# Optimization experiments

Measured on AMD Instinct MI355X. Metric: run time of the kernel, lower is better.

## Reference

```python
import jax, jax.numpy as jnp
import numpy as np

D_MODEL = 512
NUM_HEADS = 8


def setup_inputs() -> dict:
    key = jax.random.key(0)
    ks = jax.random.split(key, 12)
    B, S, D = 2, 4096, D_MODEL
    s = 1.0 / np.sqrt(D)
    return {
        "q": jax.random.normal(ks[0], (B, S, D), jnp.float32),
        "k": jax.random.normal(ks[1], (B, S, D), jnp.float32),
        "v": jax.random.normal(ks[2], (B, S, D), jnp.float32),
        "w_q": jax.random.normal(ks[3], (D, D), jnp.float32) * s,
        "b_q": jax.random.normal(ks[4], (D,), jnp.float32) * s,
        "w_k": jax.random.normal(ks[5], (D, D), jnp.float32) * s,
        "b_k": jax.random.normal(ks[6], (D,), jnp.float32) * s,
        "w_v": jax.random.normal(ks[7], (D, D), jnp.float32) * s,
        "b_v": jax.random.normal(ks[8], (D,), jnp.float32) * s,
        "w_o": jax.random.normal(ks[9], (D, D), jnp.float32) * s,
        "b_o": jax.random.normal(ks[10], (D,), jnp.float32) * s,
    }


def _split(x, num_heads):
    B, S, D = x.shape
    return x.reshape(B, S, num_heads, D // num_heads).transpose(0, 2, 1, 3)


def reference(q, k, v, w_q, b_q, w_k, b_k, w_v, b_v, w_o, b_o):
    # Linear projections (torch Linear: x @ W^T + b)
    qp = q @ w_q.T + b_q
    kp = k @ w_k.T + b_k
    vp = v @ w_v.T + b_v
    # split into heads: [B, H, S, d_head]
    qh = _split(qp, NUM_HEADS)
    kh = _split(kp, NUM_HEADS)
    vh = _split(vp, NUM_HEADS)
    d_head = qh.shape[-1]
    # NOTE: original scales by sqrt(d_model of the per-head tensor) == sqrt(d_head)
    score = jnp.einsum("bhqd,bhkd->bhqk", qh, kh) / jnp.sqrt(jnp.float32(d_head))
    attn = jax.nn.softmax(score, axis=-1)  # full [B,H,S,S] materialized, as in source
    out = jnp.einsum("bhqk,bhkd->bhqd", attn, vh)
    # concat heads back to [B, S, D]
    B, H, S, Dh = out.shape
    out = out.transpose(0, 2, 1, 3).reshape(B, S, H * Dh)
    return out @ w_o.T + b_o
```

## Files before the change

### kernel.cpp

```cpp
#include <hip/hip_runtime.h>
#include <math.h>

typedef __bf16 bf16_t;
typedef __bf16 bf16x4_v __attribute__((ext_vector_type(4)));
typedef __bf16 bf16x8_t __attribute__((ext_vector_type(8)));
typedef float f32x4_t __attribute__((ext_vector_type(4)));
typedef short short4_t __attribute__((ext_vector_type(4)));
typedef unsigned uint2_t __attribute__((ext_vector_type(2)));

#define S_LEN 4096
#define DM 512
#define NH 8
#define DH 64
#define MTOT 8192

#define Q_SCALE 0.1803368801111204f

__device__ inline f32x4_t mfma16(bf16x8_t a, bf16x8_t b, f32x4_t c) {
    return __builtin_amdgcn_mfma_f32_16x16x32_bf16(a, b, c, 0, 0, 0);
}

__device__ inline f32x4_t mfma_pv(short4_t a, short4_t b, f32x4_t c) {
    return __builtin_amdgcn_mfma_f32_16x16x16bf16_1k(a, b, c, 0, 0, 0);
}

__device__ inline unsigned pkbf16(float a, float b) {
    unsigned short ra = __builtin_bit_cast(unsigned short, (bf16_t)a);
    unsigned short rb = __builtin_bit_cast(unsigned short, (bf16_t)b);
    return (unsigned)ra | ((unsigned)rb << 16);
}

__device__ inline void async_copy16(const void* g, void* l) {
    __builtin_amdgcn_global_load_lds(
        (const __attribute__((address_space(1))) void*)g,
        (__attribute__((address_space(3))) void*)l, 16, 0, 0);
}

__global__ __launch_bounds__(256) void gemm_qkv(
    const float* __restrict__ X0, const float* __restrict__ X1, const float* __restrict__ X2,
    const float* __restrict__ W0, const float* __restrict__ W1, const float* __restrict__ W2,
    const float* __restrict__ B0, const float* __restrict__ B1, const float* __restrict__ B2,
    bf16_t* __restrict__ dst_base)
{
    const int p = blockIdx.z;
    const float* __restrict__ X  = (p == 0) ? X0 : ((p == 1) ? X1 : X2);
    const float* __restrict__ W  = (p == 0) ? W0 : ((p == 1) ? W1 : W2);
    const float* __restrict__ Bi = (p == 0) ? B0 : ((p == 1) ? B1 : B2);
    bf16_t* __restrict__ dst = dst_base + (size_t)p * (size_t)MTOT * DM;

    const int m0 = blockIdx.x * 128;
    const int n0 = blockIdx.y * 128;
    const int tid = threadIdx.x;
    const int lane = tid & 63, wid = tid >> 6;
    const int lm = lane & 15, lg = lane >> 4;
    const int wm = (wid >> 1) * 64, wn = (wid & 1) * 64;

    __shared__ bf16_t As[128][40];
    __shared__ bf16_t Bs[128][40];

    f32x4_t acc[4][4] = {};

    for (int kb = 0; kb < DM / 32; ++kb) {
        const int k0 = kb * 32;
#pragma unroll
        for (int i = 0; i < 2; ++i) {
            int idx = i * 256 + tid;
            int r = idx >> 2;
            int c = (idx & 3) * 8;
            const float* sa = X + (size_t)(m0 + r) * DM + k0 + c;
            float4 a0 = *(const float4*)sa;
            float4 a1 = *(const float4*)(sa + 4);
            bf16x8_t ha;
            ha[0] = (bf16_t)a0.x; ha[1] = (bf16_t)a0.y; ha[2] = (bf16_t)a0.z; ha[3] = (bf16_t)a0.w;
            ha[4] = (bf16_t)a1.x; ha[5] = (bf16_t)a1.y; ha[6] = (bf16_t)a1.z; ha[7] = (bf16_t)a1.w;
            *(bf16x8_t*)&As[r][c] = ha;
            const float* sb = W + (size_t)(n0 + r) * DM + k0 + c;
            float4 b0 = *(const float4*)sb;
            float4 b1 = *(const float4*)(sb + 4);
            bf16x8_t hb;
            hb[0] = (bf16_t)b0.x; hb[1] = (bf16_t)b0.y; hb[2] = (bf16_t)b0.z; hb[3] = (bf16_t)b0.w;
            hb[4] = (bf16_t)b1.x; hb[5] = (bf16_t)b1.y; hb[6] = (bf16_t)b1.z; hb[7] = (bf16_t)b1.w;
            *(bf16x8_t*)&Bs[r][c] = hb;
        }
        __syncthreads();
        bf16x8_t fa[4], fb[4];
#pragma unroll
        for (int mt = 0; mt < 4; ++mt) fa[mt] = *(bf16x8_t*)&As[wm + mt * 16 + lm][lg * 8];
#pragma unroll
        for (int nt = 0; nt < 4; ++nt) fb[nt] = *(bf16x8_t*)&Bs[wn + nt * 16 + lm][lg * 8];
#pragma unroll
        for (int mt = 0; mt < 4; ++mt)
#pragma unroll
            for (int nt = 0; nt < 4; ++nt)
                acc[mt][nt] = mfma16(fa[mt], fb[nt], acc[mt][nt]);
        __syncthreads();
    }

    if (p == 2) {
#pragma unroll
        for (int nt = 0; nt < 4; ++nt) {
            int col = n0 + wn + nt * 16 + lm;
            float bv = Bi[col];
            int h = (col >> 6) & 7, dc = col & 63;
#pragma unroll
            for (int mt = 0; mt < 4; ++mt) {
                int mrow = m0 + wm + mt * 16 + lg * 4;
                int bb = mrow >> 12, s = mrow & (S_LEN - 1);
                bf16x4_v pk;
#pragma unroll
                for (int r = 0; r < 4; ++r) pk[r] = (bf16_t)(acc[mt][nt][r] + bv);
                *(bf16x4_v*)&dst[(((size_t)(bb * NH + h)) * DH + dc) * S_LEN + s] = pk;
            }
        }
    } else {
        const float scale = (p == 0) ? Q_SCALE : 1.0f;
#pragma unroll
        for (int nt = 0; nt < 4; ++nt) {
            int col = n0 + wn + nt * 16 + lm;
            float bv = Bi[col];
            int h = (col >> 6) & 7, dc = col & 63;
#pragma unroll
            for (int mt = 0; mt < 4; ++mt) {
                int mrow = m0 + wm + mt * 16 + lg * 4;
#pragma unroll
                for (int r = 0; r < 4; ++r) {
                    int m = mrow + r;
                    int bb = m >> 12, s = m & (S_LEN - 1);
                    float vv = (acc[mt][nt][r] + bv) * scale;
                    dst[(((size_t)(bb * NH + h)) * S_LEN + s) * DH + dc] = (bf16_t)vv;
                }
            }
        }
    }
}

__global__ __launch_bounds__(512, 4) void flash_attn(
    const bf16_t* __restrict__ Qh, const bf16_t* __restrict__ Kh,
    const bf16_t* __restrict__ Vth, bf16_t* __restrict__ O)
{
    const int bh = blockIdx.y;
    const int q0 = blockIdx.x * 128;
    const int tid = threadIdx.x;
    const int lane = tid & 63, wid = tid >> 6;
    const int lm = lane & 15, lg = lane >> 4;
    const int qg = wid & 3;
    const int kvh = wid >> 2;

    const bf16_t* __restrict__ Qb  = Qh  + (size_t)bh * S_LEN * DH;
    const bf16_t* __restrict__ Kb  = Kh  + (size_t)bh * S_LEN * DH;
    const bf16_t* __restrict__ Vtg = Vth + (size_t)bh * S_LEN * DH;

    __shared__ __align__(16) char smem[35328];

    bf16x8_t bQ[2][2];
#pragma unroll
    for (int nt = 0; nt < 2; ++nt)
#pragma unroll
        for (int kd = 0; kd < 2; ++kd)
            bQ[nt][kd] = *(const bf16x8_t*)(Qb + (size_t)(q0 + qg * 32 + nt * 16 + lm) * DH + kd * 32 + lg * 8);

    f32x4_t o_acc[4][2] = {};
    float l_acc[2] = {0.f, 0.f};

    const int srow = tid >> 3;
    const int slch = (tid & 7) ^ (srow & 7);
    char* lK0 = smem + tid * 16;
    char* lK1 = smem + 8192 + tid * 16;
    char* lV0 = smem + 16384 + tid * 16;
    char* lV1 = smem + 24576 + tid * 16;
    const bf16_t* gK = Kb + (size_t)srow * DH + slch * 8;
    const bf16_t* gV = Vtg + (size_t)srow * S_LEN + slch * 8;

    const int cK0 = ((lg) ^ (lm & 7)) * 16;
    const int cK1 = ((4 + lg) ^ (lm & 7)) * 16;
    const char* ksb = smem + kvh * 8192;
    const char* vsb = smem + 16384 + kvh * 8192;

    for (int it = 0; it < S_LEN / 128; ++it) {
        const int kvb = it * 128;
        async_copy16(gK + (size_t)kvb * DH, lK0);
        async_copy16(gK + (size_t)(kvb + 64) * DH, lK1);
        async_copy16(gV + kvb, lV0);
        async_copy16(gV + kvb + 64, lV1);
        __syncthreads();

        unsigned pk[4][2][2];
#pragma unroll
        for (int mt = 0; mt < 4; ++mt) {
            const char* krow = ksb + (mt * 16 + lm) * 128;
            bf16x8_t aK0 = *(const bf16x8_t*)(krow + cK0);
            bf16x8_t aK1 = *(const bf16x8_t*)(krow + cK1);
            f32x4_t s0 = {}, s1 = {};
            s0 = mfma16(aK0, bQ[0][0], s0);
            s0 = mfma16(aK1, bQ[0][1], s0);
            s1 = mfma16(aK0, bQ[1][0], s1);
            s1 = mfma16(aK1, bQ[1][1], s1);
            float e0 = __builtin_amdgcn_exp2f(s0[0]);
            float e1 = __builtin_amdgcn_exp2f(s0[1]);
            float e2 = __builtin_amdgcn_exp2f(s0[2]);
            float e3 = __builtin_amdgcn_exp2f(s0[3]);
            pk[mt][0][0] = pkbf16(e0, e1);
            pk[mt][0][1] = pkbf16(e2, e3);
            l_acc[0] += (e0 + e1) + (e2 + e3);
            float f0 = __builtin_amdgcn_exp2f(s1[0]);
            float f1 = __builtin_amdgcn_exp2f(s1[1]);
            float f2 = __builtin_amdgcn_exp2f(s1[2]);
            float f3 = __builtin_amdgcn_exp2f(s1[3]);
            pk[mt][1][0] = pkbf16(f0, f1);
            pk[mt][1][1] = pkbf16(f2, f3);
            l_acc[1] += (f0 + f1) + (f2 + f3);
        }

#pragma unroll
        for (int mt = 0; mt < 4; ++mt) {
            const char* vrow = vsb + (mt * 16 + lm) * 128;
#pragma unroll
            for (int c = 0; c < 4; ++c) {
                int pc = (c * 2 + (lg >> 1)) ^ (lm & 7);
                short4_t vA = *(const short4_t*)(vrow + pc * 16 + (lg & 1) * 8);
                short4_t bP0 = __builtin_bit_cast(short4_t, (uint2_t){pk[c][0][0], pk[c][0][1]});
                short4_t bP1 = __builtin_bit_cast(short4_t, (uint2_t){pk[c][1][0], pk[c][1][1]});
                o_acc[mt][0] = mfma_pv(vA, bP0, o_acc[mt][0]);
                o_acc[mt][1] = mfma_pv(vA, bP1, o_acc[mt][1]);
            }
        }
        __syncthreads();
    }

#pragma unroll
    for (int nt = 0; nt < 2; ++nt) {
        l_acc[nt] += __shfl_xor(l_acc[nt], 16, 64);
        l_acc[nt] += __shfl_xor(l_acc[nt], 32, 64);
    }

    float* ob = (float*)smem + qg * (32 * 66);
    float* lb = (float*)(smem + 33792);

    if (kvh == 1) {
#pragma unroll
        for (int nt = 0; nt < 2; ++nt) {
#pragma unroll
            for (int mt = 0; mt < 4; ++mt)
#pragma unroll
                for (int r = 0; r < 4; ++r)
                    ob[(nt * 16 + lm) * 66 + mt * 16 + lg * 4 + r] = o_acc[mt][nt][r];
            if (lg == 0) lb[qg * 32 + nt * 16 + lm] = l_acc[nt];
        }
    }
    __syncthreads();
    if (kvh == 0) {
        const int bb = bh >> 3, h = bh & 7;
#pragma unroll
        for (int nt = 0; nt < 2; ++nt) {
            float ltot = l_acc[nt] + lb[qg * 32 + nt * 16 + lm];
            float inv = 1.0f / ltot;
            int q = q0 + qg * 32 + nt * 16 + lm;
            size_t base = ((size_t)(bb * S_LEN + q)) * DM + h * DH;
#pragma unroll
            for (int mt = 0; mt < 4; ++mt) {
                const float* orow = &ob[(nt * 16 + lm) * 66 + mt * 16 + lg * 4];
                bf16x4_v pkd;
#pragma unroll
                for (int r = 0; r < 4; ++r)
                    pkd[r] = (bf16_t)((o_acc[mt][nt][r] + orow[r]) * inv);
                *(bf16x4_v*)&O[base + mt * 16 + lg * 4] = pkd;
            }
        }
    }
}

__global__ __launch_bounds__(256) void gemm_out(
    const bf16_t* __restrict__ A, const float* __restrict__ W,
    const float* __restrict__ Bi, float* __restrict__ out)
{
    const int m0 = blockIdx.x * 128;
    const int n0 = blockIdx.y * 128;
    const int tid = threadIdx.x;
    const int lane = tid & 63, wid = tid >> 6;
    const int lm = lane & 15, lg = lane >> 4;
    const int wm = (wid >> 1) * 64, wn = (wid & 1) * 64;

    __shared__ bf16_t As[128][40];
    __shared__ bf16_t Bs[128][40];

    f32x4_t acc[4][4] = {};

    for (int kb = 0; kb < DM / 32; ++kb) {
        const int k0 = kb * 32;
#pragma unroll
        for (int i = 0; i < 2; ++i) {
            int idx = i * 256 + tid;
            int r = idx >> 2;
            int c = (idx & 3) * 8;
            *(bf16x8_t*)&As[r][c] = *(const bf16x8_t*)(A + (size_t)(m0 + r) * DM + k0 + c);
            const float* sb = W + (size_t)(n0 + r) * DM + k0 + c;
            float4 b0 = *(const float4*)sb;
            float4 b1 = *(const float4*)(sb + 4);
            bf16x8_t hb;
            hb[0] = (bf16_t)b0.x; hb[1] = (bf16_t)b0.y; hb[2] = (bf16_t)b0.z; hb[3] = (bf16_t)b0.w;
            hb[4] = (bf16_t)b1.x; hb[5] = (bf16_t)b1.y; hb[6] = (bf16_t)b1.z; hb[7] = (bf16_t)b1.w;
            *(bf16x8_t*)&Bs[r][c] = hb;
        }
        __syncthreads();
        bf16x8_t fa[4], fb[4];
#pragma unroll
        for (int mt = 0; mt < 4; ++mt) fa[mt] = *(bf16x8_t*)&As[wm + mt * 16 + lm][lg * 8];
#pragma unroll
        for (int nt = 0; nt < 4; ++nt) fb[nt] = *(bf16x8_t*)&Bs[wn + nt * 16 + lm][lg * 8];
#pragma unroll
        for (int mt = 0; mt < 4; ++mt)
#pragma unroll
            for (int nt = 0; nt < 4; ++nt)
                acc[mt][nt] = mfma16(fa[mt], fb[nt], acc[mt][nt]);
        __syncthreads();
    }

#pragma unroll
    for (int nt = 0; nt < 4; ++nt) {
        int col = n0 + wn + nt * 16 + lm;
        float bv = Bi[col];
#pragma unroll
        for (int mt = 0; mt < 4; ++mt) {
            int mrow = m0 + wm + mt * 16 + lg * 4;
#pragma unroll
            for (int r = 0; r < 4; ++r)
                out[(size_t)(mrow + r) * DM + col] = acc[mt][nt][r] + bv;
        }
    }
}

extern "C" void kernel_launch(void* const* d_in, const int* in_sizes, int n_in,
                              void* d_out, int out_size, void* d_ws, size_t ws_size,
                              hipStream_t stream)
{
    const float* q  = (const float*)d_in[0];
    const float* k  = (const float*)d_in[1];
    const float* v  = (const float*)d_in[2];
    const float* wq = (const float*)d_in[3];
    const float* bq = (const float*)d_in[4];
    const float* wk = (const float*)d_in[5];
    const float* bk = (const float*)d_in[6];
    const float* wv = (const float*)d_in[7];
    const float* bv = (const float*)d_in[8];
    const float* wo = (const float*)d_in[9];
    const float* bo = (const float*)d_in[10];
    float* out = (float*)d_out;

    bf16_t* ws = (bf16_t*)d_ws;
    const size_t REG = (size_t)MTOT * DM;
    bf16_t* Qh  = ws;
    bf16_t* Kh  = ws + REG;
    bf16_t* VTh = ws + 2 * REG;
    bf16_t* Ob  = ws + 3 * REG;

    dim3 g1(MTOT / 128, DM / 128, 3);
    gemm_qkv<<<g1, 256, 0, stream>>>(q, k, v, wq, wk, wv, bq, bk, bv, Qh);

    dim3 g2(S_LEN / 128, 2 * NH, 1);
    flash_attn<<<g2, 512, 0, stream>>>(Qh, Kh, VTh, Ob);

    dim3 g3(MTOT / 128, DM / 128, 1);
    gemm_out<<<g3, 256, 0, stream>>>(Ob, wo, bo, out);
}
```

Measured before the change: 255.0 us.

## Pre-convert inputs and weights to bf16 and use async LDS loads in GEMMs

```diff
diff --git a/kernel.cpp b/kernel.cpp
--- a/kernel.cpp
+++ b/kernel.cpp
@@ -16,6 +16,12 @@
 
 #define Q_SCALE 0.1803368801111204f
 
+#define REG   4194304
+#define WREG  262144
+#define W_OFF (3 * REG)
+#define CVT_TOTAL (3 * REG + 4 * WREG)
+#define QH_OFF CVT_TOTAL
+
 __device__ inline f32x4_t mfma16(bf16x8_t a, bf16x8_t b, f32x4_t c) {
     return __builtin_amdgcn_mfma_f32_16x16x32_bf16(a, b, c, 0, 0, 0);
 }
@@ -36,17 +42,40 @@
         (__attribute__((address_space(3))) void*)l, 16, 0, 0);
 }
 
+__global__ __launch_bounds__(256) void cvt_all(
+    const float* __restrict__ q, const float* __restrict__ k, const float* __restrict__ v,
+    const float* __restrict__ wq, const float* __restrict__ wk,
+    const float* __restrict__ wv, const float* __restrict__ wo,
+    bf16_t* __restrict__ dst)
+{
+    long gidx = (long)blockIdx.x * 2048 + (long)threadIdx.x * 8;
+    const float* src;
+    long off = gidx;
+    if      (gidx < 1L * REG)          { src = q; }
+    else if (gidx < 2L * REG)          { src = k;  off = gidx - 1L * REG; }
+    else if (gidx < 3L * REG)          { src = v;  off = gidx - 2L * REG; }
+    else if (gidx < W_OFF + 1L * WREG) { src = wq; off = gidx - W_OFF; }
+    else if (gidx < W_OFF + 2L * WREG) { src = wk; off = gidx - (W_OFF + 1L * WREG); }
+    else if (gidx < W_OFF + 3L * WREG) { src = wv; off = gidx - (W_OFF + 2L * WREG); }
+    else                               { src = wo; off = gidx - (W_OFF + 3L * WREG); }
+    float4 a = *(const float4*)(src + off);
+    float4 b = *(const float4*)(src + off + 4);
+    bf16x8_t h;
+    h[0] = (bf16_t)a.x; h[1] = (bf16_t)a.y; h[2] = (bf16_t)a.z; h[3] = (bf16_t)a.w;
+    h[4] = (bf16_t)b.x; h[5] = (bf16_t)b.y; h[6] = (bf16_t)b.z; h[7] = (bf16_t)b.w;
+    *(bf16x8_t*)(dst + gidx) = h;
+}
+
 __global__ __launch_bounds__(256) void gemm_qkv(
-    const float* __restrict__ X0, const float* __restrict__ X1, const float* __restrict__ X2,
-    const float* __restrict__ W0, const float* __restrict__ W1, const float* __restrict__ W2,
+    const bf16_t* __restrict__ XWb,
     const float* __restrict__ B0, const float* __restrict__ B1, const float* __restrict__ B2,
     bf16_t* __restrict__ dst_base)
 {
     const int p = blockIdx.z;
-    const float* __restrict__ X  = (p == 0) ? X0 : ((p == 1) ? X1 : X2);
-    const float* __restrict__ W  = (p == 0) ? W0 : ((p == 1) ? W1 : W2);
+    const bf16_t* __restrict__ X = XWb + (size_t)p * REG;
+    const bf16_t* __restrict__ W = XWb + W_OFF + (size_t)p * WREG;
     const float* __restrict__ Bi = (p == 0) ? B0 : ((p == 1) ? B1 : B2);
-    bf16_t* __restrict__ dst = dst_base + (size_t)p * (size_t)MTOT * DM;
+    bf16_t* __restrict__ dst = dst_base + (size_t)p * REG;
 
     const int m0 = blockIdx.x * 128;
     const int n0 = blockIdx.y * 128;
@@ -55,44 +84,40 @@
     const int lm = lane & 15, lg = lane >> 4;
     const int wm = (wid >> 1) * 64, wn = (wid & 1) * 64;
 
-    __shared__ bf16_t As[128][40];
-    __shared__ bf16_t Bs[128][40];
+    __shared__ __align__(16) bf16_t As[128 * 64];
+    __shared__ __align__(16) bf16_t Bs[128 * 64];
 
     f32x4_t acc[4][4] = {};
 
-    for (int kb = 0; kb < DM / 32; ++kb) {
-        const int k0 = kb * 32;
-#pragma unroll
-        for (int i = 0; i < 2; ++i) {
-            int idx = i * 256 + tid;
-            int r = idx >> 2;
-            int c = (idx & 3) * 8;
-            const float* sa = X + (size_t)(m0 + r) * DM + k0 + c;
-            float4 a0 = *(const float4*)sa;
-            float4 a1 = *(const float4*)(sa + 4);
-            bf16x8_t ha;
-            ha[0] = (bf16_t)a0.x; ha[1] = (bf16_t)a0.y; ha[2] = (bf16_t)a0.z; ha[3] = (bf16_t)a0.w;
-            ha[4] = (bf16_t)a1.x; ha[5] = (bf16_t)a1.y; ha[6] = (bf16_t)a1.z; ha[7] = (bf16_t)a1.w;
-            *(bf16x8_t*)&As[r][c] = ha;
-            const float* sb = W + (size_t)(n0 + r) * DM + k0 + c;
-            float4 b0 = *(const float4*)sb;
-            float4 b1 = *(const float4*)(sb + 4);
-            bf16x8_t hb;
-            hb[0] = (bf16_t)b0.x; hb[1] = (bf16_t)b0.y; hb[2] = (bf16_t)b0.z; hb[3] = (bf16_t)b0.w;
-            hb[4] = (bf16_t)b1.x; hb[5] = (bf16_t)b1.y; hb[6] = (bf16_t)b1.z; hb[7] = (bf16_t)b1.w;
-            *(bf16x8_t*)&Bs[r][c] = hb;
-        }
-        __syncthreads();
-        bf16x8_t fa[4], fb[4];
-#pragma unroll
-        for (int mt = 0; mt < 4; ++mt) fa[mt] = *(bf16x8_t*)&As[wm + mt * 16 + lm][lg * 8];
-#pragma unroll
-        for (int nt = 0; nt < 4; ++nt) fb[nt] = *(bf16x8_t*)&Bs[wn + nt * 16 + lm][lg * 8];
-#pragma unroll
-        for (int mt = 0; mt < 4; ++mt)
-#pragma unroll
-            for (int nt = 0; nt < 4; ++nt)
-                acc[mt][nt] = mfma16(fa[mt], fb[nt], acc[mt][nt]);
+    const int r0 = tid >> 3, c7 = tid & 7;
+    const int cA0 = ((lg) ^ (lm & 7)) * 8;
+    const int cA1 = ((4 + lg) ^ (lm & 7)) * 8;
+
+    for (int kb = 0; kb < DM / 64; ++kb) {
+        const int k0 = kb * 64;
+#pragma unroll
+        for (int i = 0; i < 4; ++i) {
+            int row = i * 32 + r0;
+            int ch = c7 ^ (row & 7);
+            async_copy16(X + (size_t)(m0 + row) * DM + k0 + ch * 8, (char*)As + (i * 256 + tid) * 16);
+            async_copy16(W + (size_t)(n0 + row) * DM + k0 + ch * 8, (char*)Bs + (i * 256 + tid) * 16);
+        }
+        __syncthreads();
+#pragma unroll
+        for (int kd = 0; kd < 2; ++kd) {
+            const int co = kd ? cA1 : cA0;
+            bf16x8_t fa[4], fb[4];
+#pragma unroll
+            for (int mt = 0; mt < 4; ++mt) {
+                fa[mt] = *(const bf16x8_t*)(As + (wm + mt * 16 + lm) * 64 + co);
+                fb[mt] = *(const bf16x8_t*)(Bs + (wn + mt * 16 + lm) * 64 + co);
+            }
+#pragma unroll
+            for (int mt = 0; mt < 4; ++mt)
+#pragma unroll
+                for (int nt = 0; nt < 4; ++nt)
+                    acc[mt][nt] = mfma16(fa[mt], fb[nt], acc[mt][nt]);
+        }
         __syncthreads();
     }
 
@@ -270,7 +295,7 @@
 }
 
 __global__ __launch_bounds__(256) void gemm_out(
-    const bf16_t* __restrict__ A, const float* __restrict__ W,
+    const bf16_t* __restrict__ A, const bf16_t* __restrict__ W,
     const float* __restrict__ Bi, float* __restrict__ out)
 {
     const int m0 = blockIdx.x * 128;
@@ -280,38 +305,40 @@
     const int lm = lane & 15, lg = lane >> 4;
     const int wm = (wid >> 1) * 64, wn = (wid & 1) * 64;
 
-    __shared__ bf16_t As[128][40];
-    __shared__ bf16_t Bs[128][40];
+    __shared__ __align__(16) bf16_t As[128 * 64];
+    __shared__ __align__(16) bf16_t Bs[128 * 64];
 
     f32x4_t acc[4][4] = {};
 
-    for (int kb = 0; kb < DM / 32; ++kb) {
-        const int k0 = kb * 32;
-#pragma unroll
-        for (int i = 0; i < 2; ++i) {
-            int idx = i * 256 + tid;
-            int r = idx >> 2;
-            int c = (idx & 3) * 8;
-            *(bf16x8_t*)&As[r][c] = *(const bf16x8_t*)(A + (size_t)(m0 + r) * DM + k0 + c);
-            const float* sb = W + (size_t)(n0 + r) * DM + k0 + c;
-            float4 b0 = *(const float4*)sb;
-            float4 b1 = *(const float4*)(sb + 4);
-            bf16x8_t hb;
-            hb[0] = (bf16_t)b0.x; hb[1] = (bf16_t)b0.y; hb[2] = (bf16_t)b0.z; hb[3] = (bf16_t)b0.w;
-            hb[4] = (bf16_t)b1.x; hb[5] = (bf16_t)b1.y; hb[6] = (bf16_t)b1.z; hb[7] = (bf16_t)b1.w;
-            *(bf16x8_t*)&Bs[r][c] = hb;
-        }
-        __syncthreads();
-        bf16x8_t fa[4], fb[4];
-#pragma unroll
-        for (int mt = 0; mt < 4; ++mt) fa[mt] = *(bf16x8_t*)&As[wm + mt * 16 + lm][lg * 8];
-#pragma unroll
-        for (int nt = 0; nt < 4; ++nt) fb[nt] = *(bf16x8_t*)&Bs[wn + nt * 16 + lm][lg * 8];
-#pragma unroll
-        for (int mt = 0; mt < 4; ++mt)
-#pragma unroll
-            for (int nt = 0; nt < 4; ++nt)
-                acc[mt][nt] = mfma16(fa[mt], fb[nt], acc[mt][nt]);
+    const int r0 = tid >> 3, c7 = tid & 7;
+    const int cA0 = ((lg) ^ (lm & 7)) * 8;
+    const int cA1 = ((4 + lg) ^ (lm & 7)) * 8;
+
+    for (int kb = 0; kb < DM / 64; ++kb) {
+        const int k0 = kb * 64;
+#pragma unroll
+        for (int i = 0; i < 4; ++i) {
+            int row = i * 32 + r0;
+            int ch = c7 ^ (row & 7);
+            async_copy16(A + (size_t)(m0 + row) * DM + k0 + ch * 8, (char*)As + (i * 256 + tid) * 16);
+            async_copy16(W + (size_t)(n0 + row) * DM + k0 + ch * 8, (char*)Bs + (i * 256 + tid) * 16);
+        }
+        __syncthreads();
+#pragma unroll
+        for (int kd = 0; kd < 2; ++kd) {
+            const int co = kd ? cA1 : cA0;
+            bf16x8_t fa[4], fb[4];
+#pragma unroll
+            for (int mt = 0; mt < 4; ++mt) {
+                fa[mt] = *(const bf16x8_t*)(As + (wm + mt * 16 + lm) * 64 + co);
+                fb[mt] = *(const bf16x8_t*)(Bs + (wn + mt * 16 + lm) * 64 + co);
+            }
+#pragma unroll
+            for (int mt = 0; mt < 4; ++mt)
+#pragma unroll
+                for (int nt = 0; nt < 4; ++nt)
+                    acc[mt][nt] = mfma16(fa[mt], fb[nt], acc[mt][nt]);
+        }
         __syncthreads();
     }
 
@@ -347,18 +374,21 @@
     float* out = (float*)d_out;
 
     bf16_t* ws = (bf16_t*)d_ws;
-    const size_t REG = (size_t)MTOT * DM;
-    bf16_t* Qh  = ws;
-    bf16_t* Kh  = ws + REG;
-    bf16_t* VTh = ws + 2 * REG;
-    bf16_t* Ob  = ws + 3 * REG;
+    bf16_t* XWb = ws;
+    bf16_t* Qh  = ws + QH_OFF;
+    bf16_t* Kh  = Qh + REG;
+    bf16_t* VTh = Kh + REG;
+    bf16_t* Ob  = ws;
+    bf16_t* Wob = ws + W_OFF + 3 * (size_t)WREG;
+
+    cvt_all<<<CVT_TOTAL / 2048, 256, 0, stream>>>(q, k, v, wq, wk, wv, wo, XWb);
 
     dim3 g1(MTOT / 128, DM / 128, 3);
-    gemm_qkv<<<g1, 256, 0, stream>>>(q, k, v, wq, wk, wv, bq, bk, bv, Qh);
+    gemm_qkv<<<g1, 256, 0, stream>>>(XWb, bq, bk, bv, Qh);
 
     dim3 g2(S_LEN / 128, 2 * NH, 1);
     flash_attn<<<g2, 512, 0, stream>>>(Qh, Kh, VTh, Ob);
 
     dim3 g3(MTOT / 128, DM / 128, 1);
-    gemm_out<<<g3, 256, 0, stream>>>(Ob, wo, bo, out);
-}
+    gemm_out<<<g3, 256, 0, stream>>>(Ob, Wob, bo, out);
+}
```

Measured after the change: 240.2 us. 1.06x faster.
